# Performance work log

Hardware: AMD Instinct MI355X
Metric: run time of the kernel (lower is better)

## Reference

```python
import jax, jax.numpy as jnp
import numpy as np

N_NODES = 100000
N_EDGES = 640000
EMB = 128
BATCH = 16384
N_REL = 2
HIDDEN = [128, 64, 32]
LN_EPS = 1e-5
NORM_EPS = 1e-12


def setup_inputs() -> dict:
    key = jax.random.key(0)
    ks = jax.random.split(key, 24)
    inp = {}
    inp["user_indices"] = jax.random.randint(ks[0], (BATCH,), 0, N_NODES)
    inp["item_indices"] = jax.random.randint(ks[1], (BATCH,), 0, N_NODES)
    inp["edge_index"] = jax.random.randint(ks[2], (2, N_EDGES), 0, N_NODES)
    inp["edge_type"] = jax.random.randint(ks[3], (N_EDGES,), 0, N_REL)
    inp["edge_weight"] = jax.random.uniform(ks[4], (N_EDGES,), dtype=jnp.float32)
    # parameters
    s = 1.0 / np.sqrt(EMB)
    inp["embedding"] = jax.random.normal(ks[5], (N_NODES, EMB), jnp.float32) * 0.02
    inp["w1_rel"] = jax.random.normal(ks[6], (N_REL, EMB, EMB), jnp.float32) * s
    inp["w1_root"] = jax.random.normal(ks[7], (EMB, EMB), jnp.float32) * s
    inp["b1"] = jnp.zeros((EMB,), jnp.float32)
    inp["ln_g"] = jnp.ones((EMB,), jnp.float32)
    inp["ln_b"] = jnp.zeros((EMB,), jnp.float32)
    inp["w2_rel"] = jax.random.normal(ks[8], (N_REL, EMB, EMB), jnp.float32) * s
    inp["w2_root"] = jax.random.normal(ks[9], (EMB, EMB), jnp.float32) * s
    inp["b2"] = jnp.zeros((EMB,), jnp.float32)
    dims = [2 * EMB] + HIDDEN
    for i in range(len(HIDDEN)):
        inp[f"mlp_w{i}"] = jax.random.normal(ks[10 + i], (dims[i], dims[i + 1]), jnp.float32) / np.sqrt(dims[i])
        inp[f"mlp_b{i}"] = jnp.zeros((dims[i + 1],), jnp.float32)
    d_out = HIDDEN[-1] + EMB
    inp["out_w"] = jax.random.normal(ks[20], (d_out, 1), jnp.float32) / np.sqrt(d_out)
    inp["out_b"] = jnp.zeros((1,), jnp.float32)
    return inp


def rgcn_layer(x, edge_index, edge_type, edge_weight, w_rel, w_root, bias):
    # x: [N, D]; edge_index: [2, E]; per-relation linear on gathered source feats,
    # weighted scatter-add into destination nodes, plus root transform + bias.
    src, dst = edge_index[0], edge_index[1]
    x_j = x[src]  # [E, D] gather
    msg = jnp.zeros((x_j.shape[0], w_rel.shape[2]), x.dtype)
    for r in range(w_rel.shape[0]):  # small fixed relation count
        msg = msg + jnp.where((edge_type == r)[:, None], x_j @ w_rel[r], 0.0)
    msg = msg * edge_weight[:, None]
    agg = jax.ops.segment_sum(msg, dst, num_segments=x.shape[0])
    return agg + x @ w_root + bias


def layer_norm(x, g, b):
    mu = jnp.mean(x, axis=-1, keepdims=True)
    var = jnp.mean(jnp.square(x - mu), axis=-1, keepdims=True)
    return (x - mu) * jax.lax.rsqrt(var + LN_EPS) * g + b


def l2_normalize(x):
    n = jnp.sqrt(jnp.sum(jnp.square(x), axis=-1, keepdims=True))
    return x / jnp.maximum(n, NORM_EPS)


def reference(user_indices, item_indices, edge_index, edge_type, edge_weight,
              embedding, w1_rel, w1_root, b1, ln_g, ln_b, w2_rel, w2_root, b2,
              mlp_w0, mlp_b0, mlp_w1, mlp_b1, mlp_w2, mlp_b2, out_w, out_b):
    x = embedding  # embedding(arange(N)) == full table
    x = rgcn_layer(x, edge_index, edge_type, edge_weight, w1_rel, w1_root, b1)
    x = jax.nn.relu(x)
    # dropout is identity in eval mode
    x = layer_norm(x, ln_g, ln_b)
    x = rgcn_layer(x, edge_index, edge_type, edge_weight, w2_rel, w2_root, b2)

    u = x[user_indices]  # [B, D]
    v = x[item_indices]
    gmf = l2_normalize(u) * l2_normalize(v)  # [B, D]
    h = jnp.concatenate([u, v], axis=-1)  # [B, 2D]
    for w, b in ((mlp_w0, mlp_b0), (mlp_w1, mlp_b1), (mlp_w2, mlp_b2)):
        h = jax.nn.relu(h @ w + b)
    final = jnp.concatenate([gmf, h], axis=-1)  # [B, D + 32]
    score = jax.nn.sigmoid(final @ out_w + out_b)
    return jnp.squeeze(score, axis=-1)
```

## Files before the change

kernel.cpp:

```cpp
#include <hip/hip_runtime.h>
#include <cstddef>
#include <cstdint>

#define N_NODES 100000
#define N_EDGES 640000
#define EMBD    128
#define NBATCH  16384
#define CHUNK   1024
#define NCHUNK  ((N_NODES + CHUNK - 1) / CHUNK)

typedef short bf16x8 __attribute__((ext_vector_type(8)));
typedef float f32x4  __attribute__((ext_vector_type(4)));

__device__ __forceinline__ unsigned pack_split(float x) {
    unsigned u  = __float_as_uint(x);
    unsigned hi = (u + 0x7fffu + ((u >> 16) & 1u)) & 0xffff0000u;
    float    lo = x - __uint_as_float(hi);
    unsigned ul = __float_as_uint(lo);
    unsigned lw = ((ul + 0x7fffu + ((ul >> 16) & 1u)) >> 16) & 0xffffu;
    return hi | lw;
}
__device__ __forceinline__ float unpack_split(unsigned u) {
    return __uint_as_float(u & 0xffff0000u) + __uint_as_float(u << 16);
}
__device__ __forceinline__ float bf2f(unsigned short h) {
    return __uint_as_float((unsigned)h << 16);
}

__global__ __launch_bounds__(256) void pack_hist(
    const float* __restrict__ emb, unsigned* __restrict__ xp,
    unsigned short* __restrict__ xh,
    const int* __restrict__ ei, int* __restrict__ cursor,
    const int* __restrict__ ui, const int* __restrict__ vi,
    int* __restrict__ flag, int* __restrict__ nlist, int* __restrict__ count,
    int n2, int E)
{
    const int j = blockIdx.x * 256 + threadIdx.x;
    if (j < n2) {
        const float2 v = ((const float2*)emb)[j];
        const unsigned p0 = pack_split(v.x);
        const unsigned p1 = pack_split(v.y);
        ((uint2*)xp)[j] = make_uint2(p0, p1);
        if (xh) ((unsigned*)xh)[j] = (p0 >> 16) | (p1 & 0xffff0000u);
    }
    if (j < E) atomicAdd(&cursor[ei[E + j]], 1);
    if (flag && j < 2 * NBATCH) {
        const int idx = (j < NBATCH) ? ui[j] : vi[j - NBATCH];
        if (atomicExch(&flag[idx], 1) == 0)
            nlist[atomicAdd(count, 1)] = idx;
    }
}

__global__ __launch_bounds__(256) void scan_local(
    int* __restrict__ cursor, int* __restrict__ bsum, int n)
{
    __shared__ int part[256];
    const int t    = threadIdx.x;
    const int base = blockIdx.x * CHUNK + t * 4;
    int v[4];
    int s = 0;
#pragma unroll
    for (int i = 0; i < 4; ++i) {
        const int idx = base + i;
        v[i] = (idx < n) ? cursor[idx] : 0;
        s += v[i];
    }
    part[t] = s;
    __syncthreads();
    for (int off = 1; off < 256; off <<= 1) {
        const int add = (t >= off) ? part[t - off] : 0;
        __syncthreads();
        part[t] += add;
        __syncthreads();
    }
    if (t == 255) bsum[blockIdx.x] = part[255];
    int run = (t == 0) ? 0 : part[t - 1];
#pragma unroll
    for (int i = 0; i < 4; ++i) {
        const int idx = base + i;
        if (idx < n) { cursor[idx] = run; run += v[i]; }
    }
}

__global__ __launch_bounds__(256) void scan_add(
    int* __restrict__ cursor, const int* __restrict__ bsum, int n)
{
    __shared__ int red[256];
    const int t = threadIdx.x;
    const int b = blockIdx.x;
    red[t] = (t < b && t < NCHUNK) ? bsum[t] : 0;
    __syncthreads();
    for (int off = 128; off > 0; off >>= 1) {
        if (t < off) red[t] += red[t + off];
        __syncthreads();
    }
    const int off_ = red[0];
    const int base = b * CHUNK + t * 4;
#pragma unroll
    for (int i = 0; i < 4; ++i) {
        const int idx = base + i;
        if (idx < n) cursor[idx] += off_;
    }
}

__global__ __launch_bounds__(256) void bucket_kernel(
    const int* __restrict__ ei, const int* __restrict__ et,
    const float* __restrict__ ew, int* __restrict__ cursor,
    int2* __restrict__ srec, int E)
{
    const int e = blockIdx.x * 256 + threadIdx.x;
    if (e >= E) return;
    const int src = ei[e];
    const int dst = ei[E + e];
    const int r   = et[e];
    const int pos = atomicAdd(&cursor[dst], 1);
    srec[pos] = make_int2(src | (r << 17), __float_as_int(ew[e]));
}

__device__ __forceinline__ void accum_node(
    const unsigned short* __restrict__ xh, const int2* __restrict__ srec,
    const int* __restrict__ cursor, unsigned* __restrict__ Ap,
    int wid, int lane, int N)
{
    const int s = (wid == 0) ? 0 : cursor[wid - 1];
    const int e = cursor[wid];

    float ax = 0.f, ay = 0.f, bx = 0.f, by = 0.f;
    int i = s;
    for (; i + 3 < e; i += 4) {
        const int2 r0 = srec[i];
        const int2 r1 = srec[i + 1];
        const int2 r2 = srec[i + 2];
        const int2 r3 = srec[i + 3];
        const unsigned g0 = ((const unsigned*)(xh + (size_t)(r0.x & 0x1FFFF) * EMBD))[lane];
        const unsigned g1 = ((const unsigned*)(xh + (size_t)(r1.x & 0x1FFFF) * EMBD))[lane];
        const unsigned g2 = ((const unsigned*)(xh + (size_t)(r2.x & 0x1FFFF) * EMBD))[lane];
        const unsigned g3 = ((const unsigned*)(xh + (size_t)(r3.x & 0x1FFFF) * EMBD))[lane];
        const float w0 = __int_as_float(r0.y);
        const float w1 = __int_as_float(r1.y);
        const float w2 = __int_as_float(r2.y);
        const float w3 = __int_as_float(r3.y);
        {
            const float vx = bf2f((unsigned short)(g0 & 0xffffu));
            const float vy = bf2f((unsigned short)(g0 >> 16));
            if (r0.x & (1 << 17)) { bx += vx * w0; by += vy * w0; }
            else                  { ax += vx * w0; ay += vy * w0; }
        }
        {
            const float vx = bf2f((unsigned short)(g1 & 0xffffu));
            const float vy = bf2f((unsigned short)(g1 >> 16));
            if (r1.x & (1 << 17)) { bx += vx * w1; by += vy * w1; }
            else                  { ax += vx * w1; ay += vy * w1; }
        }
        {
            const float vx = bf2f((unsigned short)(g2 & 0xffffu));
            const float vy = bf2f((unsigned short)(g2 >> 16));
            if (r2.x & (1 << 17)) { bx += vx * w2; by += vy * w2; }
            else                  { ax += vx * w2; ay += vy * w2; }
        }
        {
            const float vx = bf2f((unsigned short)(g3 & 0xffffu));
            const float vy = bf2f((unsigned short)(g3 >> 16));
            if (r3.x & (1 << 17)) { bx += vx * w3; by += vy * w3; }
            else                  { ax += vx * w3; ay += vy * w3; }
        }
    }
    for (; i < e; ++i) {
        const int2 r0 = srec[i];
        const unsigned g0 = ((const unsigned*)(xh + (size_t)(r0.x & 0x1FFFF) * EMBD))[lane];
        const float w0 = __int_as_float(r0.y);
        const float vx = bf2f((unsigned short)(g0 & 0xffffu));
        const float vy = bf2f((unsigned short)(g0 >> 16));
        if (r0.x & (1 << 17)) { bx += vx * w0; by += vy * w0; }
        else                  { ax += vx * w0; ay += vy * w0; }
    }
    ((uint2*)(Ap + (size_t)wid * EMBD))[lane]       = make_uint2(pack_split(ax), pack_split(ay));
    ((uint2*)(Ap + ((size_t)N + wid) * EMBD))[lane] = make_uint2(pack_split(bx), pack_split(by));
}

__global__ __launch_bounds__(256) void accum_csr(
    const unsigned short* __restrict__ xh, const int2* __restrict__ srec,
    const int* __restrict__ cursor, unsigned* __restrict__ Ap, int N)
{
    const int wid = blockIdx.x * 4 + (threadIdx.x >> 6);
    accum_node(xh, srec, cursor, Ap, wid, threadIdx.x & 63, N);
}

__global__ __launch_bounds__(256) void accum_csr_list(
    const unsigned short* __restrict__ xh, const int2* __restrict__ srec,
    const int* __restrict__ cursor, const int* __restrict__ nlist,
    const int* __restrict__ count, unsigned* __restrict__ Ap, int N)
{
    const int wi = blockIdx.x * 4 + (threadIdx.x >> 6);
    if (wi >= *count) return;
    accum_node(xh, srec, cursor, Ap, nlist[wi], threadIdx.x & 63, N);
}

__global__ __launch_bounds__(256) void accum_csr_full(
    const unsigned* __restrict__ xp, const int2* __restrict__ srec,
    const int* __restrict__ cursor, unsigned* __restrict__ Ap, int N)
{
    const int wid  = blockIdx.x * 4 + (threadIdx.x >> 6);
    const int lane = threadIdx.x & 63;
    const int s = (wid == 0) ? 0 : cursor[wid - 1];
    const int e = cursor[wid];
    float ax = 0.f, ay = 0.f, bx = 0.f, by = 0.f;
    for (int i = s; i < e; ++i) {
        const int2 r0 = srec[i];
        const uint2 g = ((const uint2*)(xp + (size_t)(r0.x & 0x1FFFF) * EMBD))[lane];
        const float w0 = __int_as_float(r0.y);
        const float vx = unpack_split(g.x), vy = unpack_split(g.y);
        if (r0.x & (1 << 17)) { bx += vx * w0; by += vy * w0; }
        else                  { ax += vx * w0; ay += vy * w0; }
    }
    ((uint2*)(Ap + (size_t)wid * EMBD))[lane]       = make_uint2(pack_split(ax), pack_split(ay));
    ((uint2*)(Ap + ((size_t)N + wid) * EMBD))[lane] = make_uint2(pack_split(bx), pack_split(by));
}

__global__ __launch_bounds__(256) void gemm_mfma(
    const unsigned* __restrict__ S0, const unsigned* __restrict__ S1,
    const unsigned* __restrict__ S2,
    const float* __restrict__ wrel, const float* __restrict__ wroot,
    const float* __restrict__ bias, const float* __restrict__ lng,
    const float* __restrict__ lnb, void* __restrict__ outv,
    unsigned short* __restrict__ ohi,
    const int* __restrict__ rowlist, const int* __restrict__ rowcnt,
    int M, int do_ln)
{
    __shared__ unsigned short AsH[128 * 40], AsL[128 * 40];
    __shared__ unsigned short BsH[128 * 40], BsL[128 * 40];
    __shared__ float lnbuf[2][128][2];
    __shared__ int rows[128];

    const int t    = threadIdx.x;
    const int wave = t >> 6;
    const int lane = t & 63;
    const int q    = lane >> 4;
    const int n    = lane & 15;
    const int wrow = wave & 1;
    const int wcol = wave >> 1;
    const int m0   = blockIdx.x * 128;

    const int cnt = rowcnt ? *rowcnt : M;
    if (m0 >= cnt) return;
    if (t < 128) {
        const int rr = m0 + t;
        rows[t] = (rr < cnt) ? (rowlist ? rowlist[rr] : rr) : -1;
    }
    __syncthreads();

    const int arow  = t >> 1;
    const int ahalf = t & 1;
    const int bcol  = t & 127;
    const int bkh   = t >> 7;

    f32x4 acc[4][4];
#pragma unroll
    for (int rt = 0; rt < 4; ++rt)
#pragma unroll
        for (int ct = 0; ct < 4; ++ct)
            acc[rt][ct] = (f32x4){0.f, 0.f, 0.f, 0.f};

    uint4 au0, au1, au2, au3;
    auto loadA = [&](int kc) {
        const unsigned* Sp = (kc < 4) ? S0 : (kc < 8) ? S1 : S2;
        const int node = rows[arow];
        if (node >= 0) {
            const unsigned* p = Sp + (size_t)node * EMBD + (kc & 3) * 32 + ahalf * 16;
            au0 = *(const uint4*)(p);
            au1 = *(const uint4*)(p + 4);
            au2 = *(const uint4*)(p + 8);
            au3 = *(const uint4*)(p + 12);
        } else {
            au0 = au1 = au2 = au3 = make_uint4(0u, 0u, 0u, 0u);
        }
    };

    loadA(0);

    for (int kc = 0; kc < 12; ++kc) {
        __syncthreads();

        {
            const unsigned uu[16] = {au0.x, au0.y, au0.z, au0.w,
                                     au1.x, au1.y, au1.z, au1.w,
                                     au2.x, au2.y, au2.z, au2.w,
                                     au3.x, au3.y, au3.z, au3.w};
            unsigned dh[8], dl[8];
#pragma unroll
            for (int i = 0; i < 8; ++i) {
                const unsigned e0 = uu[2 * i], e1 = uu[2 * i + 1];
                dh[i] = (e1 & 0xffff0000u) | (e0 >> 16);
                dl[i] = (e1 << 16) | (e0 & 0xffffu);
            }
            uint4* pH = (uint4*)(AsH + arow * 40 + ahalf * 16);
            uint4* pL = (uint4*)(AsL + arow * 40 + ahalf * 16);
            pH[0] = make_uint4(dh[0], dh[1], dh[2], dh[3]);
            pH[1] = make_uint4(dh[4], dh[5], dh[6], dh[7]);
            pL[0] = make_uint4(dl[0], dl[1], dl[2], dl[3]);
            pL[1] = make_uint4(dl[4], dl[5], dl[6], dl[7]);
        }

        if (kc < 11) loadA(kc + 1);

        {
            const float* Wsrc = (kc < 8) ? (wrel + (size_t)kc * 32 * EMBD)
                                         : (wroot + (size_t)(kc - 8) * 32 * EMBD);
            unsigned pk[16];
#pragma unroll
            for (int j = 0; j < 16; ++j)
                pk[j] = pack_split(Wsrc[(size_t)(bkh * 16 + j) * EMBD + bcol]);
            unsigned dh[8], dl[8];
#pragma unroll
            for (int i = 0; i < 8; ++i) {
                const unsigned e0 = pk[2 * i], e1 = pk[2 * i + 1];
                dh[i] = (e1 & 0xffff0000u) | (e0 >> 16);
                dl[i] = (e1 << 16) | (e0 & 0xffffu);
            }
            uint4* pH = (uint4*)(BsH + bcol * 40 + bkh * 16);
            uint4* pL = (uint4*)(BsL + bcol * 40 + bkh * 16);
            pH[0] = make_uint4(dh[0], dh[1], dh[2], dh[3]);
            pH[1] = make_uint4(dh[4], dh[5], dh[6], dh[7]);
            pL[0] = make_uint4(dl[0], dl[1], dl[2], dl[3]);
            pL[1] = make_uint4(dl[4], dl[5], dl[6], dl[7]);
        }
        __syncthreads();

        bf16x8 ah[4], al[4];
#pragma unroll
        for (int rt = 0; rt < 4; ++rt) {
            const int r = wrow * 64 + rt * 16 + n;
            ah[rt] = *(const bf16x8*)&AsH[r * 40 + q * 8];
            al[rt] = *(const bf16x8*)&AsL[r * 40 + q * 8];
        }
#pragma unroll
        for (int ct = 0; ct < 4; ++ct) {
            const int c = wcol * 64 + ct * 16 + n;
            const bf16x8 bh = *(const bf16x8*)&BsH[c * 40 + q * 8];
            const bf16x8 bl = *(const bf16x8*)&BsL[c * 40 + q * 8];
#pragma unroll
            for (int rt = 0; rt < 4; ++rt) {
                acc[rt][ct] = __builtin_amdgcn_mfma_f32_16x16x32_bf16(ah[rt], bh, acc[rt][ct], 0, 0, 0);
                acc[rt][ct] = __builtin_amdgcn_mfma_f32_16x16x32_bf16(ah[rt], bl, acc[rt][ct], 0, 0, 0);
                acc[rt][ct] = __builtin_amdgcn_mfma_f32_16x16x32_bf16(al[rt], bh, acc[rt][ct], 0, 0, 0);
            }
        }
    }

    float bb[4], gg[4], tb[4];
#pragma unroll
    for (int ct = 0; ct < 4; ++ct) {
        const int c = wcol * 64 + ct * 16 + n;
        bb[ct] = bias[c];
        gg[ct] = do_ln ? lng[c] : 0.f;
        tb[ct] = do_ln ? lnb[c] : 0.f;
    }

    if (do_ln) {
#pragma unroll
        for (int rt = 0; rt < 4; ++rt)
#pragma unroll
            for (int r = 0; r < 4; ++r) {
                float s = 0.f, sq = 0.f;
#pragma unroll
                for (int ct = 0; ct < 4; ++ct) {
                    float v = acc[rt][ct][r] + bb[ct];
                    v = fmaxf(v, 0.f);
                    acc[rt][ct][r] = v;
                    s += v; sq += v * v;
                }
#pragma unroll
                for (int off = 1; off < 16; off <<= 1) {
                    s  += __shfl_xor(s,  off, 64);
                    sq += __shfl_xor(sq, off, 64);
                }
                if (n == 0) {
                    const int row = wrow * 64 + rt * 16 + q * 4 + r;
                    lnbuf[wcol][row][0] = s;
                    lnbuf[wcol][row][1] = sq;
                }
            }
        __syncthreads();
        unsigned* outp = (unsigned*)outv;
#pragma unroll
        for (int rt = 0; rt < 4; ++rt)
#pragma unroll
            for (int r = 0; r < 4; ++r) {
                const int row  = wrow * 64 + rt * 16 + q * 4 + r;
                const int node = rows[row];
                const float s    = lnbuf[0][row][0] + lnbuf[1][row][0];
                const float sq   = lnbuf[0][row][1] + lnbuf[1][row][1];
                const float mu   = s * (1.0f / 128.0f);
                const float var  = sq * (1.0f / 128.0f) - mu * mu;
                const float rstd = rsqrtf(var + 1e-5f);
                if (node >= 0) {
#pragma unroll
                    for (int ct = 0; ct < 4; ++ct) {
                        const int c = wcol * 64 + ct * 16 + n;
                        const float v = (acc[rt][ct][r] - mu) * rstd * gg[ct] + tb[ct];
                        const unsigned p = pack_split(v);
                        outp[(size_t)node * EMBD + c] = p;
                        if (ohi) ohi[(size_t)node * EMBD + c] = (unsigned short)(p >> 16);
                    }
                }
            }
    } else {
        float* outp = (float*)outv;
#pragma unroll
        for (int rt = 0; rt < 4; ++rt)
#pragma unroll
            for (int r = 0; r < 4; ++r) {
                const int node = rows[wrow * 64 + rt * 16 + q * 4 + r];
                if (node >= 0) {
#pragma unroll
                    for (int ct = 0; ct < 4; ++ct) {
                        const int c = wcol * 64 + ct * 16 + n;
                        outp[(size_t)node * EMBD + c] = acc[rt][ct][r] + bb[ct];
                    }
                }
            }
    }
}

__global__ __launch_bounds__(256) void head_kernel(
    const float* __restrict__ x2, const int* __restrict__ ui, const int* __restrict__ vi,
    const float* __restrict__ mw0, const float* __restrict__ mb0,
    const float* __restrict__ mw1, const float* __restrict__ mb1,
    const float* __restrict__ mw2, const float* __restrict__ mb2,
    const float* __restrict__ ow, const float* __restrict__ ob,
    float* __restrict__ out, int B)
{
    __shared__ float h0[16][256];
    __shared__ float h1[16][128];
    __shared__ float h2[16][64];
    __shared__ float h3[16][32];
    __shared__ float ps_u[16][16], ps_v[16][16];
    __shared__ float inv_nunv[16];
    __shared__ float pg[16][16], ph[16][16];

    const int t   = threadIdx.x;
    const int bb0 = blockIdx.x * 16;

    for (int r = 0; r < 16; ++r) {
        const int b   = bb0 + r;
        const int idx = (t < 128) ? ui[b] : vi[b];
        const int c   = t & 127;
        h0[r][t] = x2[(size_t)idx * EMBD + c];
    }
    __syncthreads();

    {
        const int row = t >> 4, sub = t & 15;
        float su = 0.f, sv = 0.f;
#pragma unroll
        for (int k = 0; k < 8; ++k) {
            const float a = h0[row][sub + 16 * k];       su += a * a;
            const float b = h0[row][128 + sub + 16 * k]; sv += b * b;
        }
        ps_u[row][sub] = su; ps_v[row][sub] = sv;
    }
    __syncthreads();
    if (t < 16) {
        float su = 0.f, sv = 0.f;
#pragma unroll
        for (int k = 0; k < 16; ++k) { su += ps_u[t][k]; sv += ps_v[t][k]; }
        const float nu = fmaxf(sqrtf(su), 1e-12f);
        const float nv = fmaxf(sqrtf(sv), 1e-12f);
        inv_nunv[t] = 1.0f / (nu * nv);
    }
    __syncthreads();

    {
        const int c = t & 127, rr = t >> 7;
        float acc[8];
#pragma unroll
        for (int j = 0; j < 8; ++j) acc[j] = 0.f;
        for (int i = 0; i < 256; i += 4) {
            const float w0 = mw0[(i + 0) * 128 + c];
            const float w1 = mw0[(i + 1) * 128 + c];
            const float w2 = mw0[(i + 2) * 128 + c];
            const float w3 = mw0[(i + 3) * 128 + c];
#pragma unroll
            for (int j = 0; j < 8; ++j) {
                const float4 a = *(const float4*)&h0[rr * 8 + j][i];
                acc[j] += a.x * w0 + a.y * w1 + a.z * w2 + a.w * w3;
            }
        }
        const float bv = mb0[c];
#pragma unroll
        for (int j = 0; j < 8; ++j) h1[rr * 8 + j][c] = fmaxf(acc[j] + bv, 0.f);
    }
    __syncthreads();

    {
        const int c = t & 63, g = t >> 6;
        float acc[4] = {0.f, 0.f, 0.f, 0.f};
        for (int i = 0; i < 128; i += 4) {
            const float w0 = mw1[(i + 0) * 64 + c];
            const float w1 = mw1[(i + 1) * 64 + c];
            const float w2 = mw1[(i + 2) * 64 + c];
            const float w3 = mw1[(i + 3) * 64 + c];
#pragma unroll
            for (int j = 0; j < 4; ++j) {
                const float4 a = *(const float4*)&h1[g * 4 + j][i];
                acc[j] += a.x * w0 + a.y * w1 + a.z * w2 + a.w * w3;
            }
        }
        const float bv = mb1[c];
#pragma unroll
        for (int j = 0; j < 4; ++j) h2[g * 4 + j][c] = fmaxf(acc[j] + bv, 0.f);
    }
    __syncthreads();

    {
        const int c = t & 31, g = t >> 5;
        float acc[2] = {0.f, 0.f};
        for (int i = 0; i < 64; i += 4) {
            const float w0 = mw2[(i + 0) * 32 + c];
            const float w1 = mw2[(i + 1) * 32 + c];
            const float w2 = mw2[(i + 2) * 32 + c];
            const float w3 = mw2[(i + 3) * 32 + c];
#pragma unroll
            for (int j = 0; j < 2; ++j) {
                const float4 a = *(const float4*)&h2[g * 2 + j][i];
                acc[j] += a.x * w0 + a.y * w1 + a.z * w2 + a.w * w3;
            }
        }
        const float bv = mb2[c];
#pragma unroll
        for (int j = 0; j < 2; ++j) h3[g * 2 + j][c] = fmaxf(acc[j] + bv, 0.f);
    }
    __syncthreads();

    {
        const int row = t >> 4, sub = t & 15;
        float pgv = 0.f;
#pragma unroll
        for (int k = 0; k < 8; ++k) {
            const int c = sub + 16 * k;
            pgv += h0[row][c] * h0[row][128 + c] * ow[c];
        }
        const float phv = h3[row][sub]      * ow[128 + sub]
                        + h3[row][sub + 16] * ow[144 + sub];
        pg[row][sub] = pgv; ph[row][sub] = phv;
    }
    __syncthreads();
    if (t < 16) {
        float sg = 0.f, sh = 0.f;
#pragma unroll
        for (int k = 0; k < 16; ++k) { sg += pg[t][k]; sh += ph[t][k]; }
        const float z = sg * inv_nunv[t] + sh + ob[0];
        out[bb0 + t] = 1.0f / (1.0f + expf(-z));
    }
}

extern "C" void kernel_launch(void* const* d_in, const int* in_sizes, int n_in,
                              void* d_out, int out_size, void* d_ws, size_t ws_size,
                              hipStream_t stream)
{
    const int*   ui      = (const int*)d_in[0];
    const int*   vi      = (const int*)d_in[1];
    const int*   ei      = (const int*)d_in[2];
    const int*   et      = (const int*)d_in[3];
    const float* ew      = (const float*)d_in[4];
    const float* emb     = (const float*)d_in[5];
    const float* w1_rel  = (const float*)d_in[6];
    const float* w1_root = (const float*)d_in[7];
    const float* b1      = (const float*)d_in[8];
    const float* ln_g    = (const float*)d_in[9];
    const float* ln_b    = (const float*)d_in[10];
    const float* w2_rel  = (const float*)d_in[11];
    const float* w2_root = (const float*)d_in[12];
    const float* b2      = (const float*)d_in[13];
    const float* mw0     = (const float*)d_in[14];
    const float* mb0     = (const float*)d_in[15];
    const float* mw1     = (const float*)d_in[16];
    const float* mb1     = (const float*)d_in[17];
    const float* mw2     = (const float*)d_in[18];
    const float* mb2     = (const float*)d_in[19];
    const float* ow      = (const float*)d_in[20];
    const float* ob      = (const float*)d_in[21];
    float* out = (float*)d_out;

    const int N = N_NODES, E = N_EDGES, B = NBATCH;

    unsigned* Ap = (unsigned*)d_ws;
    unsigned* xp = Ap + (size_t)2 * N * EMBD;
    int2*   srec   = (int2*)(xp + (size_t)N * EMBD);
    int*    cursor = (int*)(srec + E);
    int*    flag   = cursor + N;
    int*    count  = flag + N;
    int*    bsum   = count + 1;
    unsigned short* xhi = (unsigned short*)(bsum + NCHUNK);
    int*    nlist  = (int*)(xhi + (size_t)N * EMBD);

    const size_t need_ext = (size_t)((char*)(nlist + 2 * NBATCH) - (char*)d_ws);
    const bool have_ext = (ws_size >= need_ext);
    unsigned short* xh = have_ext ? xhi : nullptr;

    float* x2 = (float*)Ap;

    if (have_ext) hipMemsetAsync(cursor, 0, (size_t)(2 * N + 1) * sizeof(int), stream);
    else          hipMemsetAsync(cursor, 0, (size_t)N * sizeof(int), stream);
    pack_hist<<<(N * EMBD / 2 + 255) / 256, 256, 0, stream>>>(
        emb, xp, xh, ei, cursor,
        ui, vi, have_ext ? flag : nullptr, nlist, count,
        N * EMBD / 2, E);

    scan_local<<<NCHUNK, 256, 0, stream>>>(cursor, bsum, N);
    scan_add<<<NCHUNK, 256, 0, stream>>>(cursor, bsum, N);
    bucket_kernel<<<(E + 255) / 256, 256, 0, stream>>>(ei, et, ew, cursor, srec, E);

    const int ggrid = (N + 127) / 128;

    if (have_ext) {
        accum_csr<<<N / 4, 256, 0, stream>>>(xh, srec, cursor, Ap, N);
        gemm_mfma<<<ggrid, 256, 0, stream>>>(
            Ap, Ap + (size_t)N * EMBD, xp,
            w1_rel, w1_root, b1, ln_g, ln_b, (void*)xp, xh,
            nullptr, nullptr, N, 1);

        accum_csr_list<<<(2 * NBATCH) / 4, 256, 0, stream>>>(
            xh, srec, cursor, nlist, count, Ap, N);
        gemm_mfma<<<(2 * NBATCH + 127) / 128, 256, 0, stream>>>(
            Ap, Ap + (size_t)N * EMBD, xp,
            w2_rel, w2_root, b2, nullptr, nullptr, (void*)x2, nullptr,
            nlist, count, N, 0);
    } else {
        accum_csr_full<<<N / 4, 256, 0, stream>>>(xp, srec, cursor, Ap, N);
        gemm_mfma<<<ggrid, 256, 0, stream>>>(
            Ap, Ap + (size_t)N * EMBD, xp,
            w1_rel, w1_root, b1, ln_g, ln_b, (void*)xp, nullptr,
            nullptr, nullptr, N, 1);
        accum_csr_full<<<N / 4, 256, 0, stream>>>(xp, srec, cursor, Ap, N);
        gemm_mfma<<<ggrid, 256, 0, stream>>>(
            Ap, Ap + (size_t)N * EMBD, xp,
            w2_rel, w2_root, b2, nullptr, nullptr, (void*)x2, nullptr,
            nullptr, nullptr, N, 0);
    }

    head_kernel<<<B / 16, 256, 0, stream>>>(
        x2, ui, vi, mw0, mb0, mw1, mb1, mw2, mb2, ow, ob, out, B);
}
```

Before: 427.7 us.

## Store activations as planar bf16 hi/lo and prepack weights for MFMA

Activations and aggregates are now stored as two planar bf16 arrays (high and low halves) instead of packed 32-bit split words. The GEMM can then copy A tiles straight into shared memory without per-iteration bit shuffling. Both layers' relation and root weights are split-packed once inside pack_hist into a tile-ordered layout, so each GEMM block no longer runs pack_split on the weights. The fallback path for small workspaces is removed, so the code now assumes the larger workspace is always available. The layer-2 output is also stored as split bf16, which the head kernel reassembles.

```diff
diff --git a/kernel.cpp b/kernel.cpp
--- a/kernel.cpp
+++ b/kernel.cpp
@@ -8,6 +8,7 @@
 #define NBATCH  16384
 #define CHUNK   1024
 #define NCHUNK  ((N_NODES + CHUNK - 1) / CHUNK)
+#define BELEMS  49152
 
 typedef short bf16x8 __attribute__((ext_vector_type(8)));
 typedef float f32x4  __attribute__((ext_vector_type(4)));
@@ -20,19 +21,19 @@
     unsigned lw = ((ul + 0x7fffu + ((ul >> 16) & 1u)) >> 16) & 0xffffu;
     return hi | lw;
 }
-__device__ __forceinline__ float unpack_split(unsigned u) {
-    return __uint_as_float(u & 0xffff0000u) + __uint_as_float(u << 16);
-}
 __device__ __forceinline__ float bf2f(unsigned short h) {
     return __uint_as_float((unsigned)h << 16);
 }
 
 __global__ __launch_bounds__(256) void pack_hist(
-    const float* __restrict__ emb, unsigned* __restrict__ xp,
-    unsigned short* __restrict__ xh,
+    const float* __restrict__ emb,
+    unsigned short* __restrict__ xH, unsigned short* __restrict__ xL,
     const int* __restrict__ ei, int* __restrict__ cursor,
     const int* __restrict__ ui, const int* __restrict__ vi,
     int* __restrict__ flag, int* __restrict__ nlist, int* __restrict__ count,
+    const float* __restrict__ w1rel, const float* __restrict__ w1root,
+    const float* __restrict__ w2rel, const float* __restrict__ w2root,
+    unsigned short* __restrict__ BpH, unsigned short* __restrict__ BpL,
     int n2, int E)
 {
     const int j = blockIdx.x * 256 + threadIdx.x;
@@ -40,14 +41,33 @@
         const float2 v = ((const float2*)emb)[j];
         const unsigned p0 = pack_split(v.x);
         const unsigned p1 = pack_split(v.y);
-        ((uint2*)xp)[j] = make_uint2(p0, p1);
-        if (xh) ((unsigned*)xh)[j] = (p0 >> 16) | (p1 & 0xffff0000u);
+        ((unsigned*)xH)[j] = (p1 & 0xffff0000u) | (p0 >> 16);
+        ((unsigned*)xL)[j] = (p1 << 16) | (p0 & 0xffffu);
     }
     if (j < E) atomicAdd(&cursor[ei[E + j]], 1);
-    if (flag && j < 2 * NBATCH) {
+    if (j < 2 * NBATCH) {
         const int idx = (j < NBATCH) ? ui[j] : vi[j - NBATCH];
         if (atomicExch(&flag[idx], 1) == 0)
             nlist[atomicAdd(count, 1)] = idx;
+    }
+    if (j < 2 * BELEMS) {
+        const int lay = (j >= BELEMS);
+        const int q   = j - lay * BELEMS;
+        const int p   = q >> 14;
+        const int rem = q & 16383;
+        const int k   = rem >> 7;
+        const int c   = rem & 127;
+        const float* wr = lay ? w2rel : w1rel;
+        const float* wo = lay ? w2root : w1root;
+        const float v = (p < 2) ? wr[(size_t)(p * 128 + k) * 128 + c]
+                                : wo[(size_t)k * 128 + c];
+        const unsigned ps = pack_split(v);
+        const int kc   = p * 4 + (k >> 5);
+        const int half = (k >> 4) & 1;
+        const int jj   = k & 15;
+        const size_t dst = ((size_t)(kc * 2 + half) * 128 + c) * 16 + jj;
+        BpH[(size_t)lay * BELEMS + dst] = (unsigned short)(ps >> 16);
+        BpL[(size_t)lay * BELEMS + dst] = (unsigned short)(ps & 0xffffu);
     }
 }
 
@@ -119,7 +139,8 @@
 
 __device__ __forceinline__ void accum_node(
     const unsigned short* __restrict__ xh, const int2* __restrict__ srec,
-    const int* __restrict__ cursor, unsigned* __restrict__ Ap,
+    const int* __restrict__ cursor,
+    unsigned short* __restrict__ AH, unsigned short* __restrict__ AL,
     int wid, int lane, int N)
 {
     const int s = (wid == 0) ? 0 : cursor[wid - 1];
@@ -174,56 +195,42 @@
         if (r0.x & (1 << 17)) { bx += vx * w0; by += vy * w0; }
         else                  { ax += vx * w0; ay += vy * w0; }
     }
-    ((uint2*)(Ap + (size_t)wid * EMBD))[lane]       = make_uint2(pack_split(ax), pack_split(ay));
-    ((uint2*)(Ap + ((size_t)N + wid) * EMBD))[lane] = make_uint2(pack_split(bx), pack_split(by));
+    const unsigned pax = pack_split(ax), pay = pack_split(ay);
+    const unsigned pbx = pack_split(bx), pby = pack_split(by);
+    ((unsigned*)(AH + (size_t)wid * EMBD))[lane]       = (pay & 0xffff0000u) | (pax >> 16);
+    ((unsigned*)(AL + (size_t)wid * EMBD))[lane]       = (pay << 16) | (pax & 0xffffu);
+    ((unsigned*)(AH + ((size_t)N + wid) * EMBD))[lane] = (pby & 0xffff0000u) | (pbx >> 16);
+    ((unsigned*)(AL + ((size_t)N + wid) * EMBD))[lane] = (pby << 16) | (pbx & 0xffffu);
 }
 
 __global__ __launch_bounds__(256) void accum_csr(
     const unsigned short* __restrict__ xh, const int2* __restrict__ srec,
-    const int* __restrict__ cursor, unsigned* __restrict__ Ap, int N)
+    const int* __restrict__ cursor,
+    unsigned short* __restrict__ AH, unsigned short* __restrict__ AL, int N)
 {
     const int wid = blockIdx.x * 4 + (threadIdx.x >> 6);
-    accum_node(xh, srec, cursor, Ap, wid, threadIdx.x & 63, N);
+    accum_node(xh, srec, cursor, AH, AL, wid, threadIdx.x & 63, N);
 }
 
 __global__ __launch_bounds__(256) void accum_csr_list(
     const unsigned short* __restrict__ xh, const int2* __restrict__ srec,
     const int* __restrict__ cursor, const int* __restrict__ nlist,
-    const int* __restrict__ count, unsigned* __restrict__ Ap, int N)
+    const int* __restrict__ count,
+    unsigned short* __restrict__ AH, unsigned short* __restrict__ AL, int N)
 {
     const int wi = blockIdx.x * 4 + (threadIdx.x >> 6);
     if (wi >= *count) return;
-    accum_node(xh, srec, cursor, Ap, nlist[wi], threadIdx.x & 63, N);
-}
-
-__global__ __launch_bounds__(256) void accum_csr_full(
-    const unsigned* __restrict__ xp, const int2* __restrict__ srec,
-    const int* __restrict__ cursor, unsigned* __restrict__ Ap, int N)
-{
-    const int wid  = blockIdx.x * 4 + (threadIdx.x >> 6);
-    const int lane = threadIdx.x & 63;
-    const int s = (wid == 0) ? 0 : cursor[wid - 1];
-    const int e = cursor[wid];
-    float ax = 0.f, ay = 0.f, bx = 0.f, by = 0.f;
-    for (int i = s; i < e; ++i) {
-        const int2 r0 = srec[i];
-        const uint2 g = ((const uint2*)(xp + (size_t)(r0.x & 0x1FFFF) * EMBD))[lane];
-        const float w0 = __int_as_float(r0.y);
-        const float vx = unpack_split(g.x), vy = unpack_split(g.y);
-        if (r0.x & (1 << 17)) { bx += vx * w0; by += vy * w0; }
-        else                  { ax += vx * w0; ay += vy * w0; }
-    }
-    ((uint2*)(Ap + (size_t)wid * EMBD))[lane]       = make_uint2(pack_split(ax), pack_split(ay));
-    ((uint2*)(Ap + ((size_t)N + wid) * EMBD))[lane] = make_uint2(pack_split(bx), pack_split(by));
+    accum_node(xh, srec, cursor, AH, AL, nlist[wi], threadIdx.x & 63, N);
 }
 
 __global__ __launch_bounds__(256) void gemm_mfma(
-    const unsigned* __restrict__ S0, const unsigned* __restrict__ S1,
-    const unsigned* __restrict__ S2,
-    const float* __restrict__ wrel, const float* __restrict__ wroot,
+    const unsigned short* __restrict__ S0H, const unsigned short* __restrict__ S0L,
+    const unsigned short* __restrict__ S1H, const unsigned short* __restrict__ S1L,
+    const unsigned short* __restrict__ S2H, const unsigned short* __restrict__ S2L,
+    const unsigned short* __restrict__ BpH, const unsigned short* __restrict__ BpL,
     const float* __restrict__ bias, const float* __restrict__ lng,
-    const float* __restrict__ lnb, void* __restrict__ outv,
-    unsigned short* __restrict__ ohi,
+    const float* __restrict__ lnb,
+    unsigned short* __restrict__ outH, unsigned short* __restrict__ outL,
     const int* __restrict__ rowlist, const int* __restrict__ rowcnt,
     int M, int do_ln)
 {
@@ -262,68 +269,47 @@
             acc[rt][ct] = (f32x4){0.f, 0.f, 0.f, 0.f};
 
     uint4 au0, au1, au2, au3;
+    uint4 bu0, bu1, bu2, bu3;
     auto loadA = [&](int kc) {
-        const unsigned* Sp = (kc < 4) ? S0 : (kc < 8) ? S1 : S2;
+        const unsigned short* SH = (kc < 4) ? S0H : (kc < 8) ? S1H : S2H;
+        const unsigned short* SL = (kc < 4) ? S0L : (kc < 8) ? S1L : S2L;
         const int node = rows[arow];
         if (node >= 0) {
-            const unsigned* p = Sp + (size_t)node * EMBD + (kc & 3) * 32 + ahalf * 16;
-            au0 = *(const uint4*)(p);
-            au1 = *(const uint4*)(p + 4);
-            au2 = *(const uint4*)(p + 8);
-            au3 = *(const uint4*)(p + 12);
+            const size_t off = (size_t)node * EMBD + (kc & 3) * 32 + ahalf * 16;
+            au0 = *(const uint4*)(SH + off);
+            au1 = *(const uint4*)(SH + off + 8);
+            au2 = *(const uint4*)(SL + off);
+            au3 = *(const uint4*)(SL + off + 8);
         } else {
             au0 = au1 = au2 = au3 = make_uint4(0u, 0u, 0u, 0u);
         }
     };
+    auto loadB = [&](int kc) {
+        const size_t off = ((size_t)(kc * 2 + bkh) * 128 + bcol) * 16;
+        bu0 = *(const uint4*)(BpH + off);
+        bu1 = *(const uint4*)(BpH + off + 8);
+        bu2 = *(const uint4*)(BpL + off);
+        bu3 = *(const uint4*)(BpL + off + 8);
+    };
 
     loadA(0);
+    loadB(0);
 
     for (int kc = 0; kc < 12; ++kc) {
         __syncthreads();
 
         {
-            const unsigned uu[16] = {au0.x, au0.y, au0.z, au0.w,
-                                     au1.x, au1.y, au1.z, au1.w,
-                                     au2.x, au2.y, au2.z, au2.w,
-                                     au3.x, au3.y, au3.z, au3.w};
-            unsigned dh[8], dl[8];
-#pragma unroll
-            for (int i = 0; i < 8; ++i) {
-                const unsigned e0 = uu[2 * i], e1 = uu[2 * i + 1];
-                dh[i] = (e1 & 0xffff0000u) | (e0 >> 16);
-                dl[i] = (e1 << 16) | (e0 & 0xffffu);
-            }
             uint4* pH = (uint4*)(AsH + arow * 40 + ahalf * 16);
             uint4* pL = (uint4*)(AsL + arow * 40 + ahalf * 16);
-            pH[0] = make_uint4(dh[0], dh[1], dh[2], dh[3]);
-            pH[1] = make_uint4(dh[4], dh[5], dh[6], dh[7]);
-            pL[0] = make_uint4(dl[0], dl[1], dl[2], dl[3]);
-            pL[1] = make_uint4(dl[4], dl[5], dl[6], dl[7]);
-        }
-
-        if (kc < 11) loadA(kc + 1);
-
-        {
-            const float* Wsrc = (kc < 8) ? (wrel + (size_t)kc * 32 * EMBD)
-                                         : (wroot + (size_t)(kc - 8) * 32 * EMBD);
-            unsigned pk[16];
-#pragma unroll
-            for (int j = 0; j < 16; ++j)
-                pk[j] = pack_split(Wsrc[(size_t)(bkh * 16 + j) * EMBD + bcol]);
-            unsigned dh[8], dl[8];
-#pragma unroll
-            for (int i = 0; i < 8; ++i) {
-                const unsigned e0 = pk[2 * i], e1 = pk[2 * i + 1];
-                dh[i] = (e1 & 0xffff0000u) | (e0 >> 16);
-                dl[i] = (e1 << 16) | (e0 & 0xffffu);
-            }
-            uint4* pH = (uint4*)(BsH + bcol * 40 + bkh * 16);
-            uint4* pL = (uint4*)(BsL + bcol * 40 + bkh * 16);
-            pH[0] = make_uint4(dh[0], dh[1], dh[2], dh[3]);
-            pH[1] = make_uint4(dh[4], dh[5], dh[6], dh[7]);
-            pL[0] = make_uint4(dl[0], dl[1], dl[2], dl[3]);
-            pL[1] = make_uint4(dl[4], dl[5], dl[6], dl[7]);
-        }
+            pH[0] = au0; pH[1] = au1;
+            pL[0] = au2; pL[1] = au3;
+            uint4* qH = (uint4*)(BsH + bcol * 40 + bkh * 16);
+            uint4* qL = (uint4*)(BsL + bcol * 40 + bkh * 16);
+            qH[0] = bu0; qH[1] = bu1;
+            qL[0] = bu2; qL[1] = bu3;
+        }
+
+        if (kc < 11) { loadA(kc + 1); loadB(kc + 1); }
         __syncthreads();
 
         bf16x8 ah[4], al[4];
@@ -381,7 +367,6 @@
                 }
             }
         __syncthreads();
-        unsigned* outp = (unsigned*)outv;
 #pragma unroll
         for (int rt = 0; rt < 4; ++rt)
 #pragma unroll
@@ -399,13 +384,12 @@
                         const int c = wcol * 64 + ct * 16 + n;
                         const float v = (acc[rt][ct][r] - mu) * rstd * gg[ct] + tb[ct];
                         const unsigned p = pack_split(v);
-                        outp[(size_t)node * EMBD + c] = p;
-                        if (ohi) ohi[(size_t)node * EMBD + c] = (unsigned short)(p >> 16);
+                        outH[(size_t)node * EMBD + c] = (unsigned short)(p >> 16);
+                        outL[(size_t)node * EMBD + c] = (unsigned short)(p & 0xffffu);
                     }
                 }
             }
     } else {
-        float* outp = (float*)outv;
 #pragma unroll
         for (int rt = 0; rt < 4; ++rt)
 #pragma unroll
@@ -415,7 +399,9 @@
 #pragma unroll
                     for (int ct = 0; ct < 4; ++ct) {
                         const int c = wcol * 64 + ct * 16 + n;
-                        outp[(size_t)node * EMBD + c] = acc[rt][ct][r] + bb[ct];
+                        const unsigned p = pack_split(acc[rt][ct][r] + bb[ct]);
+                        outH[(size_t)node * EMBD + c] = (unsigned short)(p >> 16);
+                        outL[(size_t)node * EMBD + c] = (unsigned short)(p & 0xffffu);
                     }
                 }
             }
@@ -423,7 +409,8 @@
 }
 
 __global__ __launch_bounds__(256) void head_kernel(
-    const float* __restrict__ x2, const int* __restrict__ ui, const int* __restrict__ vi,
+    const unsigned short* __restrict__ x2H, const unsigned short* __restrict__ x2L,
+    const int* __restrict__ ui, const int* __restrict__ vi,
     const float* __restrict__ mw0, const float* __restrict__ mb0,
     const float* __restrict__ mw1, const float* __restrict__ mb1,
     const float* __restrict__ mw2, const float* __restrict__ mb2,
@@ -445,7 +432,8 @@
         const int b   = bb0 + r;
         const int idx = (t < 128) ? ui[b] : vi[b];
         const int c   = t & 127;
-        h0[r][t] = x2[(size_t)idx * EMBD + c];
+        const size_t o = (size_t)idx * EMBD + c;
+        h0[r][t] = bf2f(x2H[o]) + bf2f(x2L[o]);
     }
     __syncthreads();
 
@@ -584,61 +572,42 @@
 
     const int N = N_NODES, E = N_EDGES, B = NBATCH;
 
-    unsigned* Ap = (unsigned*)d_ws;
-    unsigned* xp = Ap + (size_t)2 * N * EMBD;
-    int2*   srec   = (int2*)(xp + (size_t)N * EMBD);
-    int*    cursor = (int*)(srec + E);
-    int*    flag   = cursor + N;
-    int*    count  = flag + N;
-    int*    bsum   = count + 1;
-    unsigned short* xhi = (unsigned short*)(bsum + NCHUNK);
-    int*    nlist  = (int*)(xhi + (size_t)N * EMBD);
-
-    const size_t need_ext = (size_t)((char*)(nlist + 2 * NBATCH) - (char*)d_ws);
-    const bool have_ext = (ws_size >= need_ext);
-    unsigned short* xh = have_ext ? xhi : nullptr;
-
-    float* x2 = (float*)Ap;
-
-    if (have_ext) hipMemsetAsync(cursor, 0, (size_t)(2 * N + 1) * sizeof(int), stream);
-    else          hipMemsetAsync(cursor, 0, (size_t)N * sizeof(int), stream);
+    unsigned short* aggH = (unsigned short*)d_ws;
+    unsigned short* aggL = aggH + (size_t)2 * N * EMBD;
+    unsigned short* xH   = aggL + (size_t)2 * N * EMBD;
+    unsigned short* xL   = xH + (size_t)N * EMBD;
+    int2*           srec = (int2*)(xL + (size_t)N * EMBD);
+    unsigned short* BpH  = (unsigned short*)(srec + E);
+    unsigned short* BpL  = BpH + (size_t)2 * BELEMS;
+    int*            cursor = (int*)(BpL + (size_t)2 * BELEMS);
+    int*            flag   = cursor + N;
+    int*            count  = flag + N;
+    int*            bsum   = count + 1;
+    int*            nlist  = bsum + NCHUNK;
+
+    hipMemsetAsync(cursor, 0, (size_t)(2 * N + 1) * sizeof(int), stream);
     pack_hist<<<(N * EMBD / 2 + 255) / 256, 256, 0, stream>>>(
-        emb, xp, xh, ei, cursor,
-        ui, vi, have_ext ? flag : nullptr, nlist, count,
+        emb, xH, xL, ei, cursor, ui, vi, flag, nlist, count,
+        w1_rel, w1_root, w2_rel, w2_root, BpH, BpL,
         N * EMBD / 2, E);
 
     scan_local<<<NCHUNK, 256, 0, stream>>>(cursor, bsum, N);
     scan_add<<<NCHUNK, 256, 0, stream>>>(cursor, bsum, N);
     bucket_kernel<<<(E + 255) / 256, 256, 0, stream>>>(ei, et, ew, cursor, srec, E);
 
-    const int ggrid = (N + 127) / 128;
-
-    if (have_ext) {
-        accum_csr<<<N / 4, 256, 0, stream>>>(xh, srec, cursor, Ap, N);
-        gemm_mfma<<<ggrid, 256, 0, stream>>>(
-            Ap, Ap + (size_t)N * EMBD, xp,
-            w1_rel, w1_root, b1, ln_g, ln_b, (void*)xp, xh,
-            nullptr, nullptr, N, 1);
-
-        accum_csr_list<<<(2 * NBATCH) / 4, 256, 0, stream>>>(
-            xh, srec, cursor, nlist, count, Ap, N);
-        gemm_mfma<<<(2 * NBATCH + 127) / 128, 256, 0, stream>>>(
-            Ap, Ap + (size_t)N * EMBD, xp,
-            w2_rel, w2_root, b2, nullptr, nullptr, (void*)x2, nullptr,
-            nlist, count, N, 0);
-    } else {
-        accum_csr_full<<<N / 4, 256, 0, stream>>>(xp, srec, cursor, Ap, N);
-        gemm_mfma<<<ggrid, 256, 0, stream>>>(
-            Ap, Ap + (size_t)N * EMBD, xp,
-            w1_rel, w1_root, b1, ln_g, ln_b, (void*)xp, nullptr,
-            nullptr, nullptr, N, 1);
-        accum_csr_full<<<N / 4, 256, 0, stream>>>(xp, srec, cursor, Ap, N);
-        gemm_mfma<<<ggrid, 256, 0, stream>>>(
-            Ap, Ap + (size_t)N * EMBD, xp,
-            w2_rel, w2_root, b2, nullptr, nullptr, (void*)x2, nullptr,
-            nullptr, nullptr, N, 0);
-    }
+    accum_csr<<<N / 4, 256, 0, stream>>>(xH, srec, cursor, aggH, aggL, N);
+    gemm_mfma<<<(N + 127) / 128, 256, 0, stream>>>(
+        aggH, aggL, aggH + (size_t)N * EMBD, aggL + (size_t)N * EMBD, xH, xL,
+        BpH, BpL, b1, ln_g, ln_b, xH, xL,
+        nullptr, nullptr, N, 1);
+
+    accum_csr_list<<<(2 * NBATCH) / 4, 256, 0, stream>>>(
+        xH, srec, cursor, nlist, count, aggH, aggL, N);
+    gemm_mfma<<<(2 * NBATCH + 127) / 128, 256, 0, stream>>>(
+        aggH, aggL, aggH + (size_t)N * EMBD, aggL + (size_t)N * EMBD, xH, xL,
+        BpH + BELEMS, BpL + BELEMS, b2, nullptr, nullptr, xH, xL,
+        nlist, count, N, 0);
 
     head_kernel<<<B / 16, 256, 0, stream>>>(
-        x2, ui, vi, mw0, mb0, mw1, mb1, mw2, mb2, ow, ob, out, B);
-}
+        xH, xL, ui, vi, mw0, mb0, mw1, mb1, mw2, mb2, ow, ob, out, B);
+}
```

New measurement: 464.2 us. +8.5%, slower.

## Restrict layer-one computation to nodes reachable from the batch

Applied to the files above, without the earlier changes.

Marks the in-neighbors of batch-required nodes and compacts them, with the batch nodes, into a node list. Layer-one aggregation and GEMM then run only on that list instead of all nodes. This adds two small kernels, atomics and indirect row access, and also raises the GEMM kernel's occupancy hint through launch bounds. With the random graph and large batch, most nodes are likely still needed, so the skipped work may be small.

```diff
diff --git a/kernel.cpp b/kernel.cpp
--- a/kernel.cpp
+++ b/kernel.cpp
@@ -115,6 +115,40 @@
     const int r   = et[e];
     const int pos = atomicAdd(&cursor[dst], 1);
     srec[pos] = make_int2(src | (r << 17), __float_as_int(ew[e]));
+}
+
+__global__ __launch_bounds__(256) void mark_srcs(
+    const int* __restrict__ nlist, const int* __restrict__ count,
+    const int* __restrict__ cursor, const int2* __restrict__ srec,
+    int* __restrict__ flag)
+{
+    const int wi = blockIdx.x * 4 + (threadIdx.x >> 6);
+    if (wi >= *count) return;
+    const int lane = threadIdx.x & 63;
+    const int node = nlist[wi];
+    const int s = (node == 0) ? 0 : cursor[node - 1];
+    const int e = cursor[node];
+    for (int i = s + lane; i < e; i += 64)
+        atomicOr(&flag[srec[i].x & 0x1FFFF], 2);
+}
+
+__global__ __launch_bounds__(256) void build_list1(
+    const int* __restrict__ flag, int* __restrict__ nlist1,
+    int* __restrict__ count1, int n)
+{
+    const int j    = blockIdx.x * 256 + threadIdx.x;
+    const int lane = threadIdx.x & 63;
+    const bool act = (j < n) && (flag[j] != 0);
+    const unsigned long long mask = __ballot(act);
+    if (mask == 0ULL) return;
+    const int leader = __ffsll((unsigned long long)mask) - 1;
+    int base = 0;
+    if (lane == leader) base = atomicAdd(count1, __popcll(mask));
+    base = __shfl(base, leader, 64);
+    if (act) {
+        const int off = __popcll(mask & ((1ULL << lane) - 1ULL));
+        nlist1[base + off] = j;
+    }
 }
 
 __device__ __forceinline__ void accum_node(
@@ -217,7 +251,7 @@
     ((uint2*)(Ap + ((size_t)N + wid) * EMBD))[lane] = make_uint2(pack_split(bx), pack_split(by));
 }
 
-__global__ __launch_bounds__(256) void gemm_mfma(
+__global__ __launch_bounds__(256, 3) void gemm_mfma(
     const unsigned* __restrict__ S0, const unsigned* __restrict__ S1,
     const unsigned* __restrict__ S2,
     const float* __restrict__ wrel, const float* __restrict__ wroot,
@@ -590,17 +624,21 @@
     int*    cursor = (int*)(srec + E);
     int*    flag   = cursor + N;
     int*    count  = flag + N;
-    int*    bsum   = count + 1;
+    int*    count1 = count + 1;
+    int*    bsum   = count1 + 1;
     unsigned short* xhi = (unsigned short*)(bsum + NCHUNK);
     int*    nlist  = (int*)(xhi + (size_t)N * EMBD);
+    int*    nlist1 = nlist + 2 * NBATCH;
 
     const size_t need_ext = (size_t)((char*)(nlist + 2 * NBATCH) - (char*)d_ws);
+    const size_t need_l1  = (size_t)((char*)(nlist1 + N) - (char*)d_ws);
     const bool have_ext = (ws_size >= need_ext);
+    const bool have_l1  = (ws_size >= need_l1);
     unsigned short* xh = have_ext ? xhi : nullptr;
 
     float* x2 = (float*)Ap;
 
-    if (have_ext) hipMemsetAsync(cursor, 0, (size_t)(2 * N + 1) * sizeof(int), stream);
+    if (have_ext) hipMemsetAsync(cursor, 0, (size_t)(2 * N + 2) * sizeof(int), stream);
     else          hipMemsetAsync(cursor, 0, (size_t)N * sizeof(int), stream);
     pack_hist<<<(N * EMBD / 2 + 255) / 256, 256, 0, stream>>>(
         emb, xp, xh, ei, cursor,
@@ -613,13 +651,31 @@
 
     const int ggrid = (N + 127) / 128;
 
-    if (have_ext) {
+    if (have_ext && have_l1) {
+        mark_srcs<<<(2 * NBATCH) / 4, 256, 0, stream>>>(
+            nlist, count, cursor, srec, flag);
+        build_list1<<<(N + 255) / 256, 256, 0, stream>>>(
+            flag, nlist1, count1, N);
+
+        accum_csr_list<<<N / 4, 256, 0, stream>>>(
+            xh, srec, cursor, nlist1, count1, Ap, N);
+        gemm_mfma<<<ggrid, 256, 0, stream>>>(
+            Ap, Ap + (size_t)N * EMBD, xp,
+            w1_rel, w1_root, b1, ln_g, ln_b, (void*)xp, xh,
+            nlist1, count1, N, 1);
+
+        accum_csr_list<<<(2 * NBATCH) / 4, 256, 0, stream>>>(
+            xh, srec, cursor, nlist, count, Ap, N);
+        gemm_mfma<<<(2 * NBATCH + 127) / 128, 256, 0, stream>>>(
+            Ap, Ap + (size_t)N * EMBD, xp,
+            w2_rel, w2_root, b2, nullptr, nullptr, (void*)x2, nullptr,
+            nlist, count, N, 0);
+    } else if (have_ext) {
         accum_csr<<<N / 4, 256, 0, stream>>>(xh, srec, cursor, Ap, N);
         gemm_mfma<<<ggrid, 256, 0, stream>>>(
             Ap, Ap + (size_t)N * EMBD, xp,
             w1_rel, w1_root, b1, ln_g, ln_b, (void*)xp, xh,
             nullptr, nullptr, N, 1);
-
         accum_csr_list<<<(2 * NBATCH) / 4, 256, 0, stream>>>(
             xh, srec, cursor, nlist, count, Ap, N);
         gemm_mfma<<<(2 * NBATCH + 127) / 128, 256, 0, stream>>>(
```

Measured after the change: 440.4 us. 3.0% more time.
